# Performance work log

Measured on AMD Instinct MI355X. Metric: run time of the kernel, lower is better.

The kernel has to match this reference:

```python
import jax, jax.numpy as jnp
import numpy as np
from jax import lax

B, T, I, H = 128, 512, 2, 128   # batch, seq_len, input_size, hidden_size
H2 = H // 2                      # per-direction LSTM hidden


def _lstm_dir(x, Wih, Whh, bih, bhh):
    """Unidirectional LSTM over x:[B,T,in]. PyTorch gate order i,f,g,o.
    Returns (outputs [B,T,Hc], final_h [B,Hc])."""
    Hc = Whh.shape[1]
    b = bih + bhh

    def step(carry, xt):
        h, c = carry
        g = xt @ Wih.T + h @ Whh.T + b
        i, f, gg, o = jnp.split(g, 4, axis=-1)
        c = jax.nn.sigmoid(f) * c + jax.nn.sigmoid(i) * jnp.tanh(gg)
        h = jax.nn.sigmoid(o) * jnp.tanh(c)
        return (h, c), h

    h0 = jnp.zeros((x.shape[0], Hc), x.dtype)
    (hT, _), hs = lax.scan(step, (h0, h0), x.transpose(1, 0, 2))
    return hs.transpose(1, 0, 2), hT


def _bi_lstm(x, pf, pb):
    out_f, h_f = _lstm_dir(x, *pf)
    out_b, h_b = _lstm_dir(x[:, ::-1, :], *pb)
    out = jnp.concatenate([out_f, out_b[:, ::-1, :]], axis=-1)  # [B,T,H]
    hidden = jnp.concatenate([h_f, h_b], axis=-1)               # [B,H]
    return out, hidden


def _f_hid_mve(hidden_l, hidden_list, Wih, Whh, bih, bhh):
    """Custom LSTMCell scan; input = cat(hidden_list[:,t,:], hidden_l) (2H dims),
    cell size H. Collects the CELL state C each step (as in the source)."""
    Hc = Whh.shape[1]
    b = bih + bhh

    def step(carry, xt):
        h, c = carry
        g = jnp.concatenate([xt, hidden_l], axis=-1) @ Wih.T + h @ Whh.T + b
        i, f, gg, o = jnp.split(g, 4, axis=-1)
        c = jax.nn.sigmoid(f) * c + jax.nn.sigmoid(i) * jnp.tanh(gg)
        h = jax.nn.sigmoid(o) * jnp.tanh(c)
        return (h, c), c

    h0 = jnp.zeros((hidden_list.shape[0], Hc), hidden_list.dtype)
    _, cs = lax.scan(step, (h0, h0), hidden_list.transpose(1, 0, 2))
    return cs.transpose(1, 0, 2)  # [B,T,H]


def _f_hid_sim(hi, Wi, bi, Wc, bc, Wo, bo):
    C = jax.nn.sigmoid(hi @ Wi.T + bi) * jnp.tanh(hi @ Wc.T + bc)
    return jax.nn.sigmoid(hi @ Wo.T + bo) * jnp.tanh(C) + hi


def setup_inputs() -> dict:
    key = jax.random.key(0)
    ks = jax.random.split(key, 32)
    n = lambda k, s: jax.random.normal(k, s, dtype=jnp.float32) * 0.1
    inp = {}
    names = ["anchor_nearest_input", "anchor_farest_input", "nearest_input",
             "farest_input", "trajectory_anchor_input",
             "trajectory_nearest_input", "trajectory_farest_input"]
    for j, nm in enumerate(names):
        inp[nm] = jax.random.normal(ks[j], (B, T, I), dtype=jnp.float32)
    # shared bidirectional LSTM params (per-direction hidden H2)
    inp["Wih_f"] = n(ks[7], (4 * H2, I)); inp["Whh_f"] = n(ks[8], (4 * H2, H2))
    inp["bih_f"] = n(ks[9], (4 * H2,));  inp["bhh_f"] = n(ks[10], (4 * H2,))
    inp["Wih_b"] = n(ks[11], (4 * H2, I)); inp["Whh_b"] = n(ks[12], (4 * H2, H2))
    inp["bih_b"] = n(ks[13], (4 * H2,));  inp["bhh_b"] = n(ks[14], (4 * H2,))
    # f_hid_mve LSTMCell(2H -> H)
    inp["mve_Wih"] = n(ks[15], (4 * H, 2 * H)); inp["mve_Whh"] = n(ks[16], (4 * H, H))
    inp["mve_bih"] = n(ks[17], (4 * H,));       inp["mve_bhh"] = n(ks[18], (4 * H,))
    # f_hid_sim linears (H -> H)
    inp["sim_Wi"] = n(ks[19], (H, H)); inp["sim_bi"] = jnp.zeros((H,), jnp.float32)
    inp["sim_Wc"] = n(ks[20], (H, H)); inp["sim_bc"] = jnp.zeros((H,), jnp.float32)
    inp["sim_Wo"] = n(ks[21], (H, H)); inp["sim_bo"] = jnp.zeros((H,), jnp.float32)
    return inp


def reference(anchor_nearest_input, anchor_farest_input, nearest_input,
              farest_input, trajectory_anchor_input, trajectory_nearest_input,
              trajectory_farest_input,
              Wih_f, Whh_f, bih_f, bhh_f, Wih_b, Whh_b, bih_b, bhh_b,
              mve_Wih, mve_Whh, mve_bih, mve_bhh,
              sim_Wi, sim_bi, sim_Wc, sim_bc, sim_Wo, sim_bo):
    pf = (Wih_f, Whh_f, bih_f, bhh_f)
    pb = (Wih_b, Whh_b, bih_b, bhh_b)

    _, an_hidden = _bi_lstm(anchor_nearest_input, pf, pb)
    _, af_hidden = _bi_lstm(anchor_farest_input, pf, pb)
    _, n_hidden = _bi_lstm(nearest_input, pf, pb)
    _, f_hidden = _bi_lstm(farest_input, pf, pb)
    ta_out, ta_hidden = _bi_lstm(trajectory_anchor_input, pf, pb)
    tn_out, tn_hidden = _bi_lstm(trajectory_nearest_input, pf, pb)
    tf_out, tf_hidden = _bi_lstm(trajectory_farest_input, pf, pb)

    m_anchor = _f_hid_mve(ta_hidden, ta_out, mve_Wih, mve_Whh, mve_bih, mve_bhh)
    m_nearest = _f_hid_mve(tn_hidden, tn_out, mve_Wih, mve_Whh, mve_bih, mve_bhh)
    m_farest = _f_hid_mve(tf_hidden, tf_out, mve_Wih, mve_Whh, mve_bih, mve_bhh)

    sim = lambda h: _f_hid_sim(h, sim_Wi, sim_bi, sim_Wc, sim_bc, sim_Wo, sim_bo)
    an_v, af_v = sim(an_hidden), sim(af_hidden)
    n_v, f_v = sim(n_hidden), sim(f_hidden)
    t_v, tn_v, tf_v = sim(ta_hidden), sim(tn_hidden), sim(tf_hidden)

    l2 = lambda a, b: jnp.exp(-jnp.linalg.norm(a - b, ord=2, axis=-1))
    return (l2(an_v, n_v), l2(af_v, f_v), l2(t_v, tn_v), l2(t_v, tf_v),
            m_anchor, m_nearest, m_farest)
```

## Files before the change

### kernel.cpp

```cpp
#include <hip/hip_runtime.h>
#include <hip/hip_bf16.h>

#define DEV __device__ __forceinline__

constexpr int BB  = 128;
constexpr int TT  = 512;
constexpr int HH  = 128;
constexpr int H2  = 64;
constexpr int GM  = 512;

constexpr float L2E = 1.4426950408889634f;
constexpr float K2  = 2.0f * L2E;

typedef __attribute__((ext_vector_type(8))) short bf16x8;
typedef __attribute__((ext_vector_type(4))) float f32x4;

#define MFMA16(a_, b_, c_) __builtin_amdgcn_mfma_f32_16x16x32_bf16((a_), (b_), (c_), 0, 0, 0)

#define BAR_LDS() asm volatile("s_waitcnt lgkmcnt(0)\n\ts_barrier" ::: "memory")

DEV float gscale(int q) { return (q == 2) ? K2 : -L2E; }

DEV float fexp2(float x) { return __builtin_amdgcn_exp2f(x); }
DEV float rcp1p(float e) { return __builtin_amdgcn_rcpf(1.f + e); }
DEV float sigm2(float xs) { return rcp1p(fexp2(xs)); }
DEV float tanh2(float xs) { return 1.f - 2.f * rcp1p(fexp2(xs)); }

DEV unsigned short f2bf(float x) {
    __hip_bfloat16 h = __float2bfloat16(x);
    unsigned short u;
    __builtin_memcpy(&u, &h, 2);
    return u;
}
DEV float asf(unsigned int u) {
    float f;
    __builtin_memcpy(&f, &u, 4);
    return f;
}
DEV unsigned int pk2(float lo, float hi) {
    __hip_bfloat162 b2 = __float22bfloat162_rn(make_float2(lo, hi));
    unsigned int u;
    __builtin_memcpy(&u, &b2, 4);
    return u;
}
DEV f32x4 unp4(unsigned int a, unsigned int b) {
    f32x4 v;
    v[0] = asf(a << 16); v[1] = asf(a & 0xffff0000u);
    v[2] = asf(b << 16); v[3] = asf(b & 0xffff0000u);
    return v;
}
DEV bf16x8 pack8(const float* f) {
    bf16x8 v;
#pragma unroll
    for (int e = 0; e < 8; ++e) v[e] = (short)f2bf(f[e]);
    return v;
}

struct BiArgs {
    const float* x[7];
    const float* Wih[2];
    const float* Whh[2];
    const float* bih[2];
    const float* bhh[2];
    unsigned short* outs_bf;
    float* hid;
};

__global__ __launch_bounds__(512) void k_bilstm_mfma(BiArgs a) {
    const int blk  = blockIdx.x;
    const int prob = blk >> 3;
    const int b0   = (blk & 7) * 16;
    const int tid  = threadIdx.x;
    const int dir  = tid >> 8;
    const int w    = (tid >> 6) & 3;
    const int l    = tid & 63;
    const int lg   = l >> 4;
    const int lc   = l & 15;

    const float* Whh = a.Whh[dir];
    const float* Wih = a.Wih[dir];
    const float* bih = a.bih[dir];
    const float* bhh = a.bhh[dir];

    const float sw = gscale(lc & 3);
    bf16x8 wf[4][2];
#pragma unroll
    for (int mt = 0; mt < 4; ++mt) {
#pragma unroll
        for (int kh = 0; kh < 2; ++kh) {
            int orow = (lc & 3) * H2 + 16 * w + 4 * (lc >> 2) + mt;
            float tmp[8];
#pragma unroll
            for (int e = 0; e < 8; ++e)
                tmp[e] = Whh[(size_t)orow * H2 + 32 * kh + 8 * lg + e] * sw;
            wf[mt][kh] = pack8(tmp);
        }
    }
    float bia[4][4], wx0[4][4], wx1[4][4];
#pragma unroll
    for (int mt = 0; mt < 4; ++mt)
#pragma unroll
        for (int r = 0; r < 4; ++r) {
            int orow = r * H2 + 16 * w + 4 * lg + mt;
            float s = gscale(r);
            bia[mt][r] = (bih[orow] + bhh[orow]) * s;
            wx0[mt][r] = Wih[orow * 2 + 0] * s;
            wx1[mt][r] = Wih[orow * 2 + 1] * s;
        }

    __shared__ unsigned short Hb[2][2][8][16][8];
    ((unsigned long long*)&Hb[tid >> 8][0][0][0][0])[tid & 255] = 0ULL;

    const bool isTraj = (prob >= 4);
    unsigned short* outp = a.outs_bf + (size_t)(isTraj ? (prob - 4) : 0) * BB * TT * HH;
    const float2* xg2 = (const float2*)a.x[prob];
    const int c = b0 + lc;

    float cst[4] = {0.f, 0.f, 0.f, 0.f};
    int cur = 0;
    float2 xrA = xg2[(size_t)c * TT + (dir ? TT - 1 : 0)];
    float2 xrB = xg2[(size_t)c * TT + (dir ? TT - 2 : 1)];
    __syncthreads();

#define BI_BODY(XR, T_)                                                          \
    {                                                                            \
        const int t = (T_);                                                      \
        f32x4 acc[4];                                                            \
        _Pragma("unroll")                                                        \
        for (int mt = 0; mt < 4; ++mt) {                                         \
            f32x4 v;                                                             \
            _Pragma("unroll")                                                    \
            for (int r = 0; r < 4; ++r)                                          \
                v[r] = __builtin_fmaf(wx0[mt][r], XR.x,                          \
                        __builtin_fmaf(wx1[mt][r], XR.y, bia[mt][r]));           \
            acc[mt] = v;                                                         \
        }                                                                        \
        {                               \
            int tn = (t + 2 < TT) ? t + 2 : t;                                   \
            XR = xg2[(size_t)c * TT + (dir ? TT - 1 - tn : tn)];                 \
        }                                                                        \
        _Pragma("unroll")                                                        \
        for (int kh = 0; kh < 2; ++kh) {                                         \
            bf16x8 bfrag = *(const bf16x8*)&Hb[dir][cur][4 * kh + lg][lc][0];    \
            _Pragma("unroll")                                                    \
            for (int mt = 0; mt < 4; ++mt)                                       \
                acc[mt] = MFMA16(wf[mt][kh], bfrag, acc[mt]);                    \
        }                                                                        \
        const int nxt = cur ^ 1;                                                 \
        const int tcol = dir ? (TT - 1 - t) : t;                                 \
        float4 h4;                                                               \
        float* hp4 = &h4.x;                                                      \
        _Pragma("unroll")                                                        \
        for (int mt = 0; mt < 4; ++mt) {                                         \
            float si = sigm2(acc[mt][0]);                                        \
            float sf = sigm2(acc[mt][1]);                                        \
            float tg = tanh2(acc[mt][2]);                                        \
            float so = sigm2(acc[mt][3]);                                        \
            cst[mt] = sf * cst[mt] + si * tg;                                    \
            hp4[mt] = so * tanh2(K2 * cst[mt]);                                  \
        }                                                                        \
        uint2 hpk = make_uint2(pk2(h4.x, h4.y), pk2(h4.z, h4.w));                \
        {                                                                        \
            int pp = 16 * w + 4 * lg;                                            \
            *(uint2*)&Hb[dir][nxt][pp >> 3][lc][pp & 7] = hpk;                   \
        }                                                                        \
        if (isTraj)                                                              \
            *(uint2*)&outp[((size_t)c * TT + tcol) * HH + dir * H2               \
                           + 16 * w + 4 * lg] = hpk;                             \
        if (t == TT - 1)                                                         \
            *(float4*)&a.hid[((size_t)prob * BB + c) * HH + dir * H2             \
                             + 16 * w + 4 * lg] = h4;                            \
        BAR_LDS();                                                               \
        cur = nxt;                                                               \
    }

    for (int t2 = 0; t2 < TT; t2 += 2) {
        BI_BODY(xrA, t2)
        BI_BODY(xrB, t2 + 1)
    }
#undef BI_BODY
}

__global__ void k_wxB(const float* __restrict__ Wm, unsigned short* __restrict__ WxB) {
    int idx = blockIdx.x * 256 + threadIdx.x;
    int p = idx >> 7, k = idx & 127;
    int j = (p & 3) * HH + (p >> 2);
    WxB[idx] = f2bf(Wm[(size_t)j * (2 * HH) + k] * gscale(p & 3));
}

__global__ __launch_bounds__(256) void k_hp(const float* __restrict__ hidl,
                                            const float* __restrict__ Wih,
                                            const float* __restrict__ bih,
                                            const float* __restrict__ bhh,
                                            float* __restrict__ hp) {
    int traj = blockIdx.x, b = blockIdx.y;
    int j = threadIdx.x;
    __shared__ float hs[HH];
    if (j < HH) hs[j] = hidl[((size_t)traj * BB + b) * HH + j];
    __syncthreads();
    const float4* hs4 = (const float4*)hs;
#pragma unroll
    for (int rr = 0; rr < 2; ++rr) {
        int row = j + 256 * rr;
        float acc = bih[row] + bhh[row];
        const float4* w4 = (const float4*)(Wih + (size_t)row * (2 * HH) + HH);
#pragma unroll
        for (int k4 = 0; k4 < HH / 4; ++k4) {
            float4 wv = w4[k4], hv = hs4[k4];
            acc += wv.x * hv.x + wv.y * hv.y + wv.z * hv.z + wv.w * hv.w;
        }
        int p = 4 * (row & 127) + (row >> 7);
        hp[((size_t)traj * BB + b) * GM + p] = acc * gscale(row >> 7);
    }
}

__global__ __launch_bounds__(256) void k_xproj_mfma(
    const unsigned short* __restrict__ outs_bf,
    const unsigned short* __restrict__ WxB,
    const float* __restrict__ hp,
    unsigned short* __restrict__ xpb) {
    const int mb   = blockIdx.x;
    const int pb   = blockIdx.y;
    const int traj = blockIdx.z;
    const int tid  = threadIdx.x;
    const int w = tid >> 6, l = tid & 63, lg = l >> 4, lc = l & 15;
    const int m0 = mb * 128;
    const int p0 = pb * 128;
    const int c  = m0 >> 9;

    __shared__ unsigned short Xs[128 * 128];
    __shared__ unsigned short Ps[128 * 128];

    const uint4* xg4 = (const uint4*)(outs_bf + ((size_t)traj * (BB * TT) + m0) * HH);
    const uint4* pg4 = (const uint4*)(WxB + (size_t)p0 * HH);
#pragma unroll
    for (int i = 0; i < 8; ++i) {
        int j = i * 256 + tid;
        int byte = j * 16;
        int row = byte >> 8;
        int sb = byte ^ ((row & 7) << 4);
        *(uint4*)((char*)Xs + sb) = xg4[j];
        *(uint4*)((char*)Ps + sb) = pg4[j];
    }
    __syncthreads();

    bf16x8 xfrag[2][4];
#pragma unroll
    for (int xt = 0; xt < 2; ++xt)
#pragma unroll
        for (int kh = 0; kh < 4; ++kh) {
            int row = 32 * w + 16 * xt + lc;
            int byte = row * 256 + 64 * kh + 16 * lg;
            xfrag[xt][kh] = *(const bf16x8*)((const char*)Xs + (byte ^ ((row & 7) << 4)));
        }
    f32x4 acc[8][2];
#pragma unroll
    for (int pt = 0; pt < 8; ++pt)
#pragma unroll
        for (int xt = 0; xt < 2; ++xt)
#pragma unroll
            for (int r = 0; r < 4; ++r) acc[pt][xt][r] = 0.f;

#pragma unroll
    for (int pt = 0; pt < 8; ++pt) {
        bf16x8 pf[4];
#pragma unroll
        for (int kh = 0; kh < 4; ++kh) {
            int row = 16 * pt + lc;
            int byte = row * 256 + 64 * kh + 16 * lg;
            pf[kh] = *(const bf16x8*)((const char*)Ps + (byte ^ ((row & 7) << 4)));
        }
#pragma unroll
        for (int kh = 0; kh < 4; ++kh)
#pragma unroll
            for (int xt = 0; xt < 2; ++xt)
                acc[pt][xt] = MFMA16(pf[kh], xfrag[xt][kh], acc[pt][xt]);
    }
    __syncthreads();

#pragma unroll
    for (int pt = 0; pt < 8; ++pt) {
        float4 hv = *(const float4*)&hp[(((size_t)traj * BB + c)) * GM + p0 + 16 * pt + 4 * lg];
#pragma unroll
        for (int xt = 0; xt < 2; ++xt) {
            int mloc = 32 * w + 16 * xt + lc;
            int byte = mloc * 256 + (16 * pt + 4 * lg) * 2;
            uint2 u = make_uint2(pk2(acc[pt][xt][0] + hv.x, acc[pt][xt][1] + hv.y),
                                 pk2(acc[pt][xt][2] + hv.z, acc[pt][xt][3] + hv.w));
            *(uint2*)((char*)Ps + (byte ^ ((mloc & 7) << 4))) = u;
        }
    }
    __syncthreads();

    unsigned short* Cg = xpb + ((size_t)traj * (BB * TT) + m0) * GM + p0;
#pragma unroll
    for (int i = 0; i < 8; ++i) {
        int j = i * 256 + tid;
        int r = j >> 4;
        int cb = (j & 15) * 16;
        uint4 v = *(const uint4*)((const char*)Ps + ((r * 256 + cb) ^ ((r & 7) << 4)));
        *(uint4*)((char*)(Cg + (size_t)r * GM) + cb) = v;
    }
}

struct MveArgs {
    const unsigned short* xp;
    const float* Whh;
    float* mout;
};

__global__ __launch_bounds__(512) void k_mve_mfma(MveArgs a) {
    const int blk  = blockIdx.x;
    const int traj = blk >> 3;
    const int b0   = (blk & 7) * 16;
    const int tid  = threadIdx.x;
    const int w    = tid >> 6;
    const int l    = tid & 63;
    const int lg   = l >> 4;
    const int lc   = l & 15;
    const int c    = b0 + lc;

    const float sw = gscale(lc & 3);
    bf16x8 wf[4][4];
#pragma unroll
    for (int mt = 0; mt < 4; ++mt) {
#pragma unroll
        for (int kh = 0; kh < 4; ++kh) {
            int orow = (lc & 3) * HH + 16 * w + 4 * (lc >> 2) + mt;
            float tmp[8];
#pragma unroll
            for (int e = 0; e < 8; ++e)
                tmp[e] = a.Whh[(size_t)orow * HH + 32 * kh + 8 * lg + e] * sw;
            wf[mt][kh] = pack8(tmp);
        }
    }

    __shared__ unsigned short Hb[2][16][16][8];
    ((unsigned long long*)Hb)[tid] = 0ULL;

    const unsigned short* xrow = a.xp + (size_t)traj * BB * TT * GM
                               + (size_t)c * TT * GM + 64 * w + 16 * lg;
    float* mop = a.mout + (size_t)traj * BB * TT * HH
               + (size_t)c * TT * HH + 16 * w + 4 * lg;

    float cst[4] = {0.f, 0.f, 0.f, 0.f};
    int cur = 0;
    uint4 xqA0 = *(const uint4*)xrow;
    uint4 xqA1 = *(const uint4*)(xrow + 8);
    uint4 xqB0 = *(const uint4*)(xrow + GM);
    uint4 xqB1 = *(const uint4*)(xrow + GM + 8);
    __syncthreads();

#define MVE_BODY(XQ0, XQ1, T_)                                                   \
    {                                                                            \
        const int t = (T_);                                                      \
        f32x4 acc[4];                                                            \
        acc[0] = unp4(XQ0.x, XQ0.y);                                             \
        acc[1] = unp4(XQ0.z, XQ0.w);                                             \
        acc[2] = unp4(XQ1.x, XQ1.y);                                             \
        acc[3] = unp4(XQ1.z, XQ1.w);                                             \
        {                              \
            const unsigned short* pf = xrow                                      \
                + (size_t)((t + 2 < TT) ? t + 2 : t) * GM;                       \
            XQ0 = *(const uint4*)pf;                                             \
            XQ1 = *(const uint4*)(pf + 8);                                       \
        }                                                                        \
        _Pragma("unroll")                                                        \
        for (int kh = 0; kh < 4; ++kh) {                                         \
            bf16x8 bfrag = *(const bf16x8*)&Hb[cur][4 * kh + lg][lc][0];         \
            _Pragma("unroll")                                                    \
            for (int mt = 0; mt < 4; ++mt)                                       \
                acc[mt] = MFMA16(wf[mt][kh], bfrag, acc[mt]);                    \
        }                                                                        \
        const int nxt = cur ^ 1;                                                 \
        float4 cs4, h4;                                                          \
        float* cp4 = &cs4.x;                                                     \
        float* hp4 = &h4.x;                                                      \
        _Pragma("unroll")                                                        \
        for (int mt = 0; mt < 4; ++mt) {                                         \
            float si = sigm2(acc[mt][0]);                                        \
            float sf = sigm2(acc[mt][1]);                                        \
            float tg = tanh2(acc[mt][2]);                                        \
            float so = sigm2(acc[mt][3]);                                        \
            cst[mt] = sf * cst[mt] + si * tg;                                    \
            hp4[mt] = so * tanh2(K2 * cst[mt]);                                  \
            cp4[mt] = cst[mt];                                                   \
        }                                                                        \
        {                                                                        \
            int pp = 16 * w + 4 * lg;                                            \
            *(uint2*)&Hb[nxt][pp >> 3][lc][pp & 7] =                             \
                make_uint2(pk2(h4.x, h4.y), pk2(h4.z, h4.w));                    \
        }                                                                        \
        *(float4*)&mop[(size_t)t * HH] = cs4;                                    \
        BAR_LDS();                                                               \
        cur = nxt;                                                               \
    }

    for (int t2 = 0; t2 < TT; t2 += 2) {
        MVE_BODY(xqA0, xqA1, t2)
        MVE_BODY(xqB0, xqB1, t2 + 1)
    }
#undef MVE_BODY
}

__global__ __launch_bounds__(128) void k_sim(const float* __restrict__ hid,
                                             const float* __restrict__ Wi, const float* __restrict__ bi,
                                             const float* __restrict__ Wc, const float* __restrict__ bc,
                                             const float* __restrict__ Wo, const float* __restrict__ bo,
                                             float* __restrict__ simv) {
    int which = blockIdx.x >> 7;
    int b = blockIdx.x & 127;
    int j = threadIdx.x;
    __shared__ float hs[HH];
    hs[j] = hid[((size_t)which * BB + b) * HH + j];
    __syncthreads();
    float ai = bi[j], ac = bc[j], ao = bo[j];
    const float4* wi4 = (const float4*)(Wi + (size_t)j * HH);
    const float4* wc4 = (const float4*)(Wc + (size_t)j * HH);
    const float4* wo4 = (const float4*)(Wo + (size_t)j * HH);
#pragma unroll
    for (int k4 = 0; k4 < HH / 4; ++k4) {
        float4 h = ((const float4*)hs)[k4];
        float4 vi = wi4[k4]; ai += vi.x*h.x + vi.y*h.y + vi.z*h.z + vi.w*h.w;
        float4 vc = wc4[k4]; ac += vc.x*h.x + vc.y*h.y + vc.z*h.z + vc.w*h.w;
        float4 vo = wo4[k4]; ao += vo.x*h.x + vo.y*h.y + vo.z*h.z + vo.w*h.w;
    }
    float Cv = (1.f / (1.f + __expf(-ai))) * tanhf(ac);
    float v = (1.f / (1.f + __expf(-ao))) * tanhf(Cv) + hs[j];
    simv[((size_t)which * BB + b) * HH + j] = v;
}

__global__ __launch_bounds__(64) void k_l2(const float* __restrict__ simv,
                                           float* __restrict__ out) {
    int p = blockIdx.x >> 7;
    int b = blockIdx.x & 127;
    int aw, cw;
    switch (p) {
        case 0: aw = 0; cw = 2; break;
        case 1: aw = 1; cw = 3; break;
        case 2: aw = 4; cw = 5; break;
        default: aw = 4; cw = 6; break;
    }
    int l = threadIdx.x;
    const float* va = simv + ((size_t)aw * BB + b) * HH;
    const float* vc = simv + ((size_t)cw * BB + b) * HH;
    float d0 = va[l] - vc[l];
    float d1 = va[l + 64] - vc[l + 64];
    float s = d0 * d0 + d1 * d1;
#pragma unroll
    for (int m = 32; m >= 1; m >>= 1) s += __shfl_xor(s, m, 64);
    if (l == 0) out[p * BB + b] = expf(-sqrtf(s));
}

extern "C" void kernel_launch(void* const* d_in, const int* in_sizes, int n_in,
                              void* d_out_v, int out_size, void* d_ws, size_t ws_size,
                              hipStream_t stream) {
    const float* mWih  = (const float*)d_in[15];
    const float* mWhh  = (const float*)d_in[16];
    const float* mbih  = (const float*)d_in[17];
    const float* mbhh  = (const float*)d_in[18];
    const float* sWi   = (const float*)d_in[19];
    const float* sbi   = (const float*)d_in[20];
    const float* sWc   = (const float*)d_in[21];
    const float* sbc   = (const float*)d_in[22];
    const float* sWo   = (const float*)d_in[23];
    const float* sbo   = (const float*)d_in[24];

    constexpr size_t OUTSBF_LEN = (size_t)3 * BB * TT * HH;
    constexpr size_t HID_LEN    = (size_t)7 * BB * HH;
    constexpr size_t WXB_LEN    = (size_t)GM * HH;
    constexpr size_t SIMV_LEN   = HID_LEN;
    constexpr size_t HP_LEN     = (size_t)3 * BB * GM;
    constexpr size_t XP_LEN     = (size_t)3 * BB * TT * GM;

    char* ws = (char*)d_ws;
    unsigned short* outs_bf = (unsigned short*)ws;                 ws += OUTSBF_LEN * 2;
    float*          hid     = (float*)ws;                          ws += HID_LEN * 4;
    unsigned short* WxB     = (unsigned short*)ws;                 ws += WXB_LEN * 2;
    float*          simv    = (float*)ws;                          ws += SIMV_LEN * 4;
    float*          hp      = (float*)ws;                          ws += HP_LEN * 4;
    unsigned short* xpb     = (unsigned short*)ws;                 ws += XP_LEN * 2;

    float* dout = (float*)d_out_v;
    float* mout = dout + 512;

    BiArgs ba;
    for (int i = 0; i < 7; ++i) ba.x[i] = (const float*)d_in[i];
    ba.Wih[0] = (const float*)d_in[7];  ba.Whh[0] = (const float*)d_in[8];
    ba.bih[0] = (const float*)d_in[9];  ba.bhh[0] = (const float*)d_in[10];
    ba.Wih[1] = (const float*)d_in[11]; ba.Whh[1] = (const float*)d_in[12];
    ba.bih[1] = (const float*)d_in[13]; ba.bhh[1] = (const float*)d_in[14];
    ba.outs_bf = outs_bf; ba.hid = hid;

    k_wxB<<<256, 256, 0, stream>>>(mWih, WxB);
    k_bilstm_mfma<<<56, 512, 0, stream>>>(ba);
    k_hp<<<dim3(3, BB), 256, 0, stream>>>(hid + (size_t)4 * BB * HH, mWih, mbih, mbhh, hp);

    dim3 gx(BB * TT / 128, GM / 128, 3);
    k_xproj_mfma<<<gx, 256, 0, stream>>>(outs_bf, WxB, hp, xpb);

    MveArgs ma;
    ma.xp = xpb; ma.Whh = mWhh; ma.mout = mout;
    k_mve_mfma<<<24, 512, 0, stream>>>(ma);

    k_sim<<<7 * BB, 128, 0, stream>>>(hid, sWi, sbi, sWc, sbc, sWo, sbo, simv);
    k_l2<<<4 * BB, 64, 0, stream>>>(simv, dout);
}
```

Measured before the change: 920.2 us.

## Halve MVE recurrence wavefronts with wider per-wave gate tiles and permuted projection layout

The MVE recurrent kernel now runs 4 wavefronts per block instead of 8, each computing 8 M-tiles. The input-projection matrix and the precomputed hidden term are reordered so each wave loads contiguous bf16 gate pre-activations, and these are spread into MFMA accumulators by multiplying with an identity fragment instead of unpacking them with scalar ops. The wave's own previous h fragment is kept in registers rather than re-read from LDS, and the gate math merges exponentials to use fewer reciprocals. The aim is a shorter per-step critical path with a cheaper barrier over fewer waves, at the cost of more registers per thread and more MFMA work per wave.

```diff
diff --git a/kernel.cpp b/kernel.cpp
--- a/kernel.cpp
+++ b/kernel.cpp
@@ -22,7 +22,8 @@
 DEV float gscale(int q) { return (q == 2) ? K2 : -L2E; }
 
 DEV float fexp2(float x) { return __builtin_amdgcn_exp2f(x); }
-DEV float rcp1p(float e) { return __builtin_amdgcn_rcpf(1.f + e); }
+DEV float frcp(float x)  { return __builtin_amdgcn_rcpf(x); }
+DEV float rcp1p(float e) { return frcp(1.f + e); }
 DEV float sigm2(float xs) { return rcp1p(fexp2(xs)); }
 DEV float tanh2(float xs) { return 1.f - 2.f * rcp1p(fexp2(xs)); }
 
@@ -32,28 +33,21 @@
     __builtin_memcpy(&u, &h, 2);
     return u;
 }
-DEV float asf(unsigned int u) {
-    float f;
-    __builtin_memcpy(&f, &u, 4);
-    return f;
-}
 DEV unsigned int pk2(float lo, float hi) {
     __hip_bfloat162 b2 = __float22bfloat162_rn(make_float2(lo, hi));
     unsigned int u;
     __builtin_memcpy(&u, &b2, 4);
     return u;
 }
-DEV f32x4 unp4(unsigned int a, unsigned int b) {
-    f32x4 v;
-    v[0] = asf(a << 16); v[1] = asf(a & 0xffff0000u);
-    v[2] = asf(b << 16); v[3] = asf(b & 0xffff0000u);
-    return v;
-}
 DEV bf16x8 pack8(const float* f) {
     bf16x8 v;
 #pragma unroll
     for (int e = 0; e < 8; ++e) v[e] = (short)f2bf(f[e]);
     return v;
+}
+DEV int s2p(int s) {
+    int w = s >> 7, j = (s >> 5) & 3, k = s & 31, r15 = k & 15;
+    return 128 * w + 8 * j + 4 * (k >> 4) + 32 * (r15 >> 2) + (k & 3);
 }
 
 struct BiArgs {
@@ -135,7 +129,7 @@
                         __builtin_fmaf(wx1[mt][r], XR.y, bia[mt][r]));           \
             acc[mt] = v;                                                         \
         }                                                                        \
-        {                               \
+        {                                                                        \
             int tn = (t + 2 < TT) ? t + 2 : t;                                   \
             XR = xg2[(size_t)c * TT + (dir ? TT - 1 - tn : tn)];                 \
         }                                                                        \
@@ -181,11 +175,12 @@
 #undef BI_BODY
 }
 
-__global__ void k_wxB(const float* __restrict__ Wm, unsigned short* __restrict__ WxB) {
+__global__ void k_wxS(const float* __restrict__ Wm, unsigned short* __restrict__ WxB) {
     int idx = blockIdx.x * 256 + threadIdx.x;
-    int p = idx >> 7, k = idx & 127;
-    int j = (p & 3) * HH + (p >> 2);
-    WxB[idx] = f2bf(Wm[(size_t)j * (2 * HH) + k] * gscale(p & 3));
+    int s = idx >> 7, k = idx & 127;
+    int p = s2p(s);
+    int h = p >> 2, q = p & 3;
+    WxB[idx] = f2bf(Wm[(size_t)(q * HH + h) * (2 * HH) + k] * gscale(q));
 }
 
 __global__ __launch_bounds__(256) void k_hp(const float* __restrict__ hidl,
@@ -201,16 +196,18 @@
     const float4* hs4 = (const float4*)hs;
 #pragma unroll
     for (int rr = 0; rr < 2; ++rr) {
-        int row = j + 256 * rr;
-        float acc = bih[row] + bhh[row];
-        const float4* w4 = (const float4*)(Wih + (size_t)row * (2 * HH) + HH);
+        int srow = j + 256 * rr;
+        int p = s2p(srow);
+        int h = p >> 2, q = p & 3;
+        int orow = q * HH + h;
+        float acc = bih[orow] + bhh[orow];
+        const float4* w4 = (const float4*)(Wih + (size_t)orow * (2 * HH) + HH);
 #pragma unroll
         for (int k4 = 0; k4 < HH / 4; ++k4) {
             float4 wv = w4[k4], hv = hs4[k4];
             acc += wv.x * hv.x + wv.y * hv.y + wv.z * hv.z + wv.w * hv.w;
         }
-        int p = 4 * (row & 127) + (row >> 7);
-        hp[((size_t)traj * BB + b) * GM + p] = acc * gscale(row >> 7);
+        hp[((size_t)traj * BB + b) * GM + srow] = acc * gscale(q);
     }
 }
 
@@ -309,7 +306,7 @@
     float* mout;
 };
 
-__global__ __launch_bounds__(512) void k_mve_mfma(MveArgs a) {
+__global__ __launch_bounds__(256, 1) void k_mve_mfma(MveArgs a) {
     const int blk  = blockIdx.x;
     const int traj = blk >> 3;
     const int b0   = (blk & 7) * 16;
@@ -321,12 +318,12 @@
     const int c    = b0 + lc;
 
     const float sw = gscale(lc & 3);
-    bf16x8 wf[4][4];
-#pragma unroll
-    for (int mt = 0; mt < 4; ++mt) {
+    bf16x8 wf[8][4];
+#pragma unroll
+    for (int mt = 0; mt < 8; ++mt) {
 #pragma unroll
         for (int kh = 0; kh < 4; ++kh) {
-            int orow = (lc & 3) * HH + 16 * w + 4 * (lc >> 2) + mt;
+            int orow = (lc & 3) * HH + 32 * w + 8 * (lc >> 2) + mt;
             float tmp[8];
 #pragma unroll
             for (int e = 0; e < 8; ++e)
@@ -334,71 +331,92 @@
             wf[mt][kh] = pack8(tmp);
         }
     }
+    bf16x8 idlo, idhi;
+    {
+        short bufl[8] = {0,0,0,0,0,0,0,0}, bufh[8] = {0,0,0,0,0,0,0,0};
+        if (lg == (lc >> 3)) bufl[lc & 7] = (short)0x3F80;
+        if (lg == 2 + (lc >> 3)) bufh[lc & 7] = (short)0x3F80;
+        __builtin_memcpy(&idlo, bufl, 16);
+        __builtin_memcpy(&idhi, bufh, 16);
+    }
 
     __shared__ unsigned short Hb[2][16][16][8];
-    ((unsigned long long*)Hb)[tid] = 0ULL;
+    ((uint4*)Hb)[tid] = make_uint4(0, 0, 0, 0);
 
     const unsigned short* xrow = a.xp + (size_t)traj * BB * TT * GM
-                               + (size_t)c * TT * GM + 64 * w + 16 * lg;
+                               + (size_t)c * TT * GM + 128 * w + 8 * lg;
     float* mop = a.mout + (size_t)traj * BB * TT * HH
-               + (size_t)c * TT * HH + 16 * w + 4 * lg;
-
-    float cst[4] = {0.f, 0.f, 0.f, 0.f};
+               + (size_t)c * TT * HH + 32 * w + 8 * lg;
+
+    float cst[8] = {0.f, 0.f, 0.f, 0.f, 0.f, 0.f, 0.f, 0.f};
+    bf16x8 hprev = bf16x8(0);
     int cur = 0;
-    uint4 xqA0 = *(const uint4*)xrow;
-    uint4 xqA1 = *(const uint4*)(xrow + 8);
-    uint4 xqB0 = *(const uint4*)(xrow + GM);
-    uint4 xqB1 = *(const uint4*)(xrow + GM + 8);
-    __syncthreads();
-
-#define MVE_BODY(XQ0, XQ1, T_)                                                   \
+    uint4 xqA[4], xqB[4];
+#pragma unroll
+    for (int j = 0; j < 4; ++j) {
+        xqA[j] = *(const uint4*)(xrow + 32 * j);
+        xqB[j] = *(const uint4*)(xrow + GM + 32 * j);
+    }
+    __syncthreads();
+
+    const f32x4 zed = {0.f, 0.f, 0.f, 0.f};
+
+#define MVE_BODY(XQ, T_)                                                         \
     {                                                                            \
         const int t = (T_);                                                      \
-        f32x4 acc[4];                                                            \
-        acc[0] = unp4(XQ0.x, XQ0.y);                                             \
-        acc[1] = unp4(XQ0.z, XQ0.w);                                             \
-        acc[2] = unp4(XQ1.x, XQ1.y);                                             \
-        acc[3] = unp4(XQ1.z, XQ1.w);                                             \
+        f32x4 acc[8];                                                            \
+        _Pragma("unroll")                                                        \
+        for (int j = 0; j < 4; ++j) {                                            \
+            bf16x8 bq;                                                           \
+            __builtin_memcpy(&bq, &XQ[j], 16);                                   \
+            acc[2 * j]     = MFMA16(idlo, bq, zed);                              \
+            acc[2 * j + 1] = MFMA16(idhi, bq, zed);                              \
+        }                                                                        \
         {                              \
             const unsigned short* pf = xrow                                      \
                 + (size_t)((t + 2 < TT) ? t + 2 : t) * GM;                       \
-            XQ0 = *(const uint4*)pf;                                             \
-            XQ1 = *(const uint4*)(pf + 8);                                       \
+            _Pragma("unroll")                                                    \
+            for (int j = 0; j < 4; ++j) XQ[j] = *(const uint4*)(pf + 32 * j);    \
         }                                                                        \
         _Pragma("unroll")                                                        \
         for (int kh = 0; kh < 4; ++kh) {                                         \
-            bf16x8 bfrag = *(const bf16x8*)&Hb[cur][4 * kh + lg][lc][0];         \
+            bf16x8 bfrag = (kh == w) ? hprev                                     \
+                : *(const bf16x8*)&Hb[cur][4 * kh + lg][lc][0];                  \
             _Pragma("unroll")                                                    \
-            for (int mt = 0; mt < 4; ++mt)                                       \
+            for (int mt = 0; mt < 8; ++mt)                                       \
                 acc[mt] = MFMA16(wf[mt][kh], bfrag, acc[mt]);                    \
         }                                                                        \
         const int nxt = cur ^ 1;                                                 \
-        float4 cs4, h4;                                                          \
-        float* cp4 = &cs4.x;                                                     \
-        float* hp4 = &h4.x;                                                      \
+        float h8[8];                                                             \
         _Pragma("unroll")                                                        \
-        for (int mt = 0; mt < 4; ++mt) {                                         \
-            float si = sigm2(acc[mt][0]);                                        \
-            float sf = sigm2(acc[mt][1]);                                        \
-            float tg = tanh2(acc[mt][2]);                                        \
-            float so = sigm2(acc[mt][3]);                                        \
-            cst[mt] = sf * cst[mt] + si * tg;                                    \
-            hp4[mt] = so * tanh2(K2 * cst[mt]);                                  \
-            cp4[mt] = cst[mt];                                                   \
-        }                                                                        \
-        {                                                                        \
-            int pp = 16 * w + 4 * lg;                                            \
-            *(uint2*)&Hb[nxt][pp >> 3][lc][pp & 7] =                             \
-                make_uint2(pk2(h4.x, h4.y), pk2(h4.z, h4.w));                    \
-        }                                                                        \
-        *(float4*)&mop[(size_t)t * HH] = cs4;                                    \
+        for (int mt = 0; mt < 8; ++mt) {                                         \
+            float Ai = fexp2(acc[mt][0]);                             \
+            float Bg = fexp2(acc[mt][2]);                             \
+            float sf = rcp1p(fexp2(acc[mt][1]));                     \
+            float ig = (Bg - 1.f) * frcp((1.f + Ai) * (1.f + Bg));               \
+            cst[mt] = __builtin_fmaf(sf, cst[mt], ig);                           \
+            float Cc = fexp2(K2 * cst[mt]);                           \
+            float Do = fexp2(acc[mt][3]);                             \
+            h8[mt] = (Cc - 1.f) * frcp((1.f + Do) * (1.f + Cc));                 \
+        }                                                                        \
+        {                         \
+            uint4 hu = make_uint4(pk2(h8[0], h8[1]), pk2(h8[2], h8[3]),          \
+                                  pk2(h8[4], h8[5]), pk2(h8[6], h8[7]));         \
+            __builtin_memcpy(&hprev, &hu, 16);                                   \
+            *(bf16x8*)&Hb[nxt][4 * w + lg][lc][0] = hprev;                       \
+        }                                                                        \
+        {                        \
+            float* mo = mop + (size_t)t * HH;                                    \
+            *(float4*)mo       = make_float4(cst[0], cst[1], cst[2], cst[3]);    \
+            *(float4*)(mo + 4) = make_float4(cst[4], cst[5], cst[6], cst[7]);    \
+        }                                                                        \
         BAR_LDS();                                                               \
         cur = nxt;                                                               \
     }
 
     for (int t2 = 0; t2 < TT; t2 += 2) {
-        MVE_BODY(xqA0, xqA1, t2)
-        MVE_BODY(xqB0, xqB1, t2 + 1)
+        MVE_BODY(xqA, t2)
+        MVE_BODY(xqB, t2 + 1)
     }
 #undef MVE_BODY
 }
@@ -492,7 +510,7 @@
     ba.bih[1] = (const float*)d_in[13]; ba.bhh[1] = (const float*)d_in[14];
     ba.outs_bf = outs_bf; ba.hid = hid;
 
-    k_wxB<<<256, 256, 0, stream>>>(mWih, WxB);
+    k_wxS<<<256, 256, 0, stream>>>(mWih, WxB);
     k_bilstm_mfma<<<56, 512, 0, stream>>>(ba);
     k_hp<<<dim3(3, BB), 256, 0, stream>>>(hid + (size_t)4 * BB * HH, mWih, mbih, mbhh, hp);
 
@@ -501,7 +519,7 @@
 
     MveArgs ma;
     ma.xp = xpb; ma.Whh = mWhh; ma.mout = mout;
-    k_mve_mfma<<<24, 512, 0, stream>>>(ma);
+    k_mve_mfma<<<24, 256, 0, stream>>>(ma);
 
     k_sim<<<7 * BB, 128, 0, stream>>>(hid, sWi, sbi, sWc, sbc, sWo, sbo, simv);
     k_l2<<<4 * BB, 64, 0, stream>>>(simv, dout);
```

Result: slower. 971.0 us (+5.5%).
